# Kernel tuning notes

Measured on AMD Instinct MI355X. Metric: run time of the kernel, lower is better.

## Reference

```python
import jax, jax.numpy as jnp
import numpy as np

N, C, D, H, W = 4, 9, 16, 1024, 1024  # batch, grid channels, grid size, image HxW


def setup_inputs() -> dict:
    key = jax.random.key(0)
    k1, k2, k3, k4 = jax.random.split(key, 4)
    bilateral_grid = jax.random.normal(k1, (N, C, D, D, D), dtype=jnp.float32)
    guidemap = jax.random.uniform(k2, (N, 3, H, W), dtype=jnp.float32)
    conv_w = jax.random.normal(k3, (3, C + 3), dtype=jnp.float32) * 0.1  # 1x1 conv kernel
    conv_b = jax.random.normal(k4, (3,), dtype=jnp.float32) * 0.1
    return {"bilateral_grid": bilateral_grid, "guidemap": guidemap,
            "conv_w": conv_w, "conv_b": conv_b}


def _trilinear_slice(grid, guide):
    # grid: [N, C, D, D, D]; guide: [N, 3, H, W] with values in [0,1]
    n, c, d = grid.shape[0], grid.shape[1], grid.shape[2]
    h, w = guide.shape[2], guide.shape[3]
    grid_flat = grid.reshape(n, c, d * d * d)
    coords = jnp.clip(guide, 0.0, 1.0) * (d - 1)          # [N,3,H,W]
    i0 = jnp.clip(jnp.floor(coords), 0, d - 2).astype(jnp.int32)
    f = coords - i0.astype(coords.dtype)                   # fractional part
    r0, g0, b0 = i0[:, 0], i0[:, 1], i0[:, 2]              # [N,H,W]
    fr, fg, fb = f[:, 0], f[:, 1], f[:, 2]                 # [N,H,W]

    def gather(ir, ig, ib):
        flat = ((ir * d + ig) * d + ib).reshape(n, 1, h * w)
        return jnp.take_along_axis(grid_flat, flat, axis=2)  # [N,C,H*W]

    out = jnp.zeros((n, c, h * w), dtype=grid.dtype)
    for dr in (0, 1):
        for dg in (0, 1):
            for db in (0, 1):
                wgt = ((fr if dr else 1.0 - fr) *
                       (fg if dg else 1.0 - fg) *
                       (fb if db else 1.0 - fb)).reshape(n, 1, h * w)
                out = out + gather(r0 + dr, g0 + dg, b0 + db) * wgt
    return out.reshape(n, c, h, w)


def reference(bilateral_grid, guidemap, conv_w, conv_b):
    res = _trilinear_slice(bilateral_grid, guidemap)       # [N,9,H,W]
    res = jnp.concatenate([res, guidemap], axis=1)         # [N,12,H,W]
    out = jnp.einsum('oi,nihw->nohw', conv_w, res) + conv_b[None, :, None, None]
    return out
```

## Files before the change

kernel.cpp:

```cpp
#include <hip/hip_runtime.h>
#include <hip/hip_bf16.h>

static constexpr int N_ = 4;
static constexpr int C_ = 9;
static constexpr int D_ = 16;
static constexpr int HWp = 1024 * 1024;
static constexpr int CELLS = D_ * D_ * D_;
static constexpr int PT = HWp / 4;
static constexpr int TPB = 512;
static constexpr int BPI = 256;

typedef float f32x4 __attribute__((ext_vector_type(4)));

__device__ __forceinline__ void unpack3(uint2 w, float& x, float& y, float& z) {
    x = __uint_as_float(w.x << 16);
    y = __uint_as_float(w.x & 0xFFFF0000u);
    z = __uint_as_float(w.y << 16);
}

__device__ __forceinline__ float lerp1(float a, float b, float t) {
    return fmaf(b - a, t, a);
}

__global__ __launch_bounds__(256) void fold_kernel(
    const float* __restrict__ grid, const float* __restrict__ cw,
    uint2* __restrict__ folded)
{
    const int idx  = blockIdx.x * 256 + threadIdx.x;
    const int n    = idx >> 12;
    const int cell = idx & (CELLS - 1);
    const float* g = grid + (size_t)n * C_ * CELLS + cell;

    float a0 = 0.f, a1 = 0.f, a2 = 0.f;
#pragma unroll
    for (int c = 0; c < C_; ++c) {
        float v = g[(size_t)c * CELLS];
        a0 = fmaf(cw[c],      v, a0);
        a1 = fmaf(cw[12 + c], v, a1);
        a2 = fmaf(cw[24 + c], v, a2);
    }
    uint2 v;
    v.x = (unsigned)__bfloat16_as_ushort(__float2bfloat16(a0))
        | ((unsigned)__bfloat16_as_ushort(__float2bfloat16(a1)) << 16);
    v.y = (unsigned)__bfloat16_as_ushort(__float2bfloat16(a2));
    folded[idx] = v;
}

__global__ __launch_bounds__(TPB) void slice_kernel(
    const uint2* __restrict__ folded, const float* __restrict__ guide,
    const float* __restrict__ cw, const float* __restrict__ cbias,
    float* __restrict__ out)
{
    __shared__ uint2 sPre[CELLS];

    const int n  = blockIdx.x >> 8;
    const int bi = blockIdx.x & (BPI - 1);

    {
        const uint4* src = (const uint4*)(folded + (size_t)n * CELLS);
        uint4* dst = (uint4*)sPre;
#pragma unroll
        for (int k = 0; k < (CELLS / 2) / TPB; ++k) {
            int i = k * TPB + threadIdx.x;
            dst[i] = src[i];
        }
    }
    __syncthreads();

    const f32x4* gR = (const f32x4*)(guide + (size_t)(n * 3 + 0) * HWp);
    const f32x4* gG = (const f32x4*)(guide + (size_t)(n * 3 + 1) * HWp);
    const f32x4* gB = (const f32x4*)(guide + (size_t)(n * 3 + 2) * HWp);
    f32x4* oR = (f32x4*)(out + (size_t)(n * 3 + 0) * HWp);
    f32x4* oG = (f32x4*)(out + (size_t)(n * 3 + 1) * HWp);
    f32x4* oB = (f32x4*)(out + (size_t)(n * 3 + 2) * HWp);

    const float w0r = cw[9],  w0g = cw[10], w0b = cw[11];
    const float w1r = cw[21], w1g = cw[22], w1b = cw[23];
    const float w2r = cw[33], w2g = cw[34], w2b = cw[35];
    const float bi0 = cbias[0], bi1 = cbias[1], bi2 = cbias[2];

    const int base0 = bi * (PT / BPI);

#pragma unroll
    for (int it = 0; it < (PT / BPI) / TPB; ++it) {
        const int p4 = base0 + it * TPB + threadIdx.x;
        f32x4 r4 = __builtin_nontemporal_load(gR + p4);
        f32x4 g4 = __builtin_nontemporal_load(gG + p4);
        f32x4 b4 = __builtin_nontemporal_load(gB + p4);

        float rr[4] = {r4.x, r4.y, r4.z, r4.w};
        float gg[4] = {g4.x, g4.y, g4.z, g4.w};
        float bb[4] = {b4.x, b4.y, b4.z, b4.w};
        float o0[4], o1[4], o2[4];

#pragma unroll
        for (int j = 0; j < 4; ++j) {
            float cr = fminf(fmaxf(rr[j], 0.f), 1.f) * 15.f;
            float cg = fminf(fmaxf(gg[j], 0.f), 1.f) * 15.f;
            float cb = fminf(fmaxf(bb[j], 0.f), 1.f) * 15.f;
            int ir = min((int)cr, 14);
            int ig = min((int)cg, 14);
            int ib = min((int)cb, 14);
            float fr = cr - (float)ir;
            float fg = cg - (float)ig;
            float fb = cb - (float)ib;
            int base = (ir * 16 + ig) * 16 + ib;

            uint2 q000 = sPre[base];
            uint2 q001 = sPre[base + 1];
            uint2 q010 = sPre[base + 16];
            uint2 q011 = sPre[base + 17];
            uint2 q100 = sPre[base + 256];
            uint2 q101 = sPre[base + 257];
            uint2 q110 = sPre[base + 272];
            uint2 q111 = sPre[base + 273];

            float ax, ay, az, bx, by, bz;
            float v00x, v00y, v00z, v01x, v01y, v01z;
            float v10x, v10y, v10z, v11x, v11y, v11z;

            unpack3(q000, ax, ay, az); unpack3(q001, bx, by, bz);
            v00x = lerp1(ax, bx, fb); v00y = lerp1(ay, by, fb); v00z = lerp1(az, bz, fb);
            unpack3(q010, ax, ay, az); unpack3(q011, bx, by, bz);
            v01x = lerp1(ax, bx, fb); v01y = lerp1(ay, by, fb); v01z = lerp1(az, bz, fb);
            unpack3(q100, ax, ay, az); unpack3(q101, bx, by, bz);
            v10x = lerp1(ax, bx, fb); v10y = lerp1(ay, by, fb); v10z = lerp1(az, bz, fb);
            unpack3(q110, ax, ay, az); unpack3(q111, bx, by, bz);
            v11x = lerp1(ax, bx, fb); v11y = lerp1(ay, by, fb); v11z = lerp1(az, bz, fb);

            float v0x = lerp1(v00x, v01x, fg);
            float v0y = lerp1(v00y, v01y, fg);
            float v0z = lerp1(v00z, v01z, fg);
            float v1x = lerp1(v10x, v11x, fg);
            float v1y = lerp1(v10y, v11y, fg);
            float v1z = lerp1(v10z, v11z, fg);

            float vx = lerp1(v0x, v1x, fr);
            float vy = lerp1(v0y, v1y, fr);
            float vz = lerp1(v0z, v1z, fr);

            o0[j] = vx + fmaf(w0r, rr[j], fmaf(w0g, gg[j], fmaf(w0b, bb[j], bi0)));
            o1[j] = vy + fmaf(w1r, rr[j], fmaf(w1g, gg[j], fmaf(w1b, bb[j], bi1)));
            o2[j] = vz + fmaf(w2r, rr[j], fmaf(w2g, gg[j], fmaf(w2b, bb[j], bi2)));
        }

        f32x4 s0 = {o0[0], o0[1], o0[2], o0[3]};
        f32x4 s1 = {o1[0], o1[1], o1[2], o1[3]};
        f32x4 s2 = {o2[0], o2[1], o2[2], o2[3]};
        __builtin_nontemporal_store(s0, oR + p4);
        __builtin_nontemporal_store(s1, oG + p4);
        __builtin_nontemporal_store(s2, oB + p4);
    }
}

extern "C" void kernel_launch(void* const* d_in, const int* in_sizes, int n_in,
                              void* d_out, int out_size, void* d_ws, size_t ws_size,
                              hipStream_t stream) {
    const float* grid  = (const float*)d_in[0];
    const float* guide = (const float*)d_in[1];
    const float* cw    = (const float*)d_in[2];
    const float* cb    = (const float*)d_in[3];
    float* out = (float*)d_out;
    uint2* folded = (uint2*)d_ws;

    fold_kernel<<<(N_ * CELLS) / 256, 256, 0, stream>>>(grid, cw, folded);
    slice_kernel<<<N_ * BPI, TPB, 0, stream>>>(folded, guide, cw, cb, out);
}
```

Measured before the change: 115.2 us.

## Store b-axis neighbor pairs in folded grid to halve LDS gathers

The fold kernel now writes each cell together with its +1 neighbor along the b axis as one 16-byte record. The slice kernel can then fetch the 8 trilinear corners with 4 uint4 LDS reads instead of 8 uint2 reads. The shared table doubles to 64KB per block, which limits occupancy. To amortize the larger per-block table load, blocks per image drop from 256 to 128, so each block handles more pixels.

```diff
diff --git a/kernel.cpp b/kernel.cpp
--- a/kernel.cpp
+++ b/kernel.cpp
@@ -8,61 +8,79 @@
 static constexpr int CELLS = D_ * D_ * D_;
 static constexpr int PT = HWp / 4;
 static constexpr int TPB = 512;
-static constexpr int BPI = 256;
+static constexpr int BPI = 128;
 
 typedef float f32x4 __attribute__((ext_vector_type(4)));
-
-__device__ __forceinline__ void unpack3(uint2 w, float& x, float& y, float& z) {
-    x = __uint_as_float(w.x << 16);
-    y = __uint_as_float(w.x & 0xFFFF0000u);
-    z = __uint_as_float(w.y << 16);
-}
 
 __device__ __forceinline__ float lerp1(float a, float b, float t) {
     return fmaf(b - a, t, a);
 }
 
+__device__ __forceinline__ unsigned pack2bf(float a, float b) {
+    return (unsigned)__bfloat16_as_ushort(__float2bfloat16(a))
+         | ((unsigned)__bfloat16_as_ushort(__float2bfloat16(b)) << 16);
+}
+
+__device__ __forceinline__ void unpack_lerp(uint4 q, float t,
+                                            float& vx, float& vy, float& vz) {
+    float ax = __uint_as_float(q.x << 16);
+    float ay = __uint_as_float(q.x & 0xFFFF0000u);
+    float az = __uint_as_float(q.y << 16);
+    float bx = __uint_as_float(q.z << 16);
+    float by = __uint_as_float(q.z & 0xFFFF0000u);
+    float bz = __uint_as_float(q.w << 16);
+    vx = lerp1(ax, bx, t);
+    vy = lerp1(ay, by, t);
+    vz = lerp1(az, bz, t);
+}
+
 __global__ __launch_bounds__(256) void fold_kernel(
     const float* __restrict__ grid, const float* __restrict__ cw,
-    uint2* __restrict__ folded)
+    uint4* __restrict__ folded)
 {
     const int idx  = blockIdx.x * 256 + threadIdx.x;
     const int n    = idx >> 12;
     const int cell = idx & (CELLS - 1);
-    const float* g = grid + (size_t)n * C_ * CELLS + cell;
+    const int cellN = ((cell & 15) < 15) ? cell + 1 : cell;
+    const float* g = grid + (size_t)n * C_ * CELLS;
 
     float a0 = 0.f, a1 = 0.f, a2 = 0.f;
+    float c0 = 0.f, c1 = 0.f, c2 = 0.f;
 #pragma unroll
     for (int c = 0; c < C_; ++c) {
-        float v = g[(size_t)c * CELLS];
+        float v = g[(size_t)c * CELLS + cell];
+        float w = g[(size_t)c * CELLS + cellN];
         a0 = fmaf(cw[c],      v, a0);
         a1 = fmaf(cw[12 + c], v, a1);
         a2 = fmaf(cw[24 + c], v, a2);
+        c0 = fmaf(cw[c],      w, c0);
+        c1 = fmaf(cw[12 + c], w, c1);
+        c2 = fmaf(cw[24 + c], w, c2);
     }
-    uint2 v;
-    v.x = (unsigned)__bfloat16_as_ushort(__float2bfloat16(a0))
-        | ((unsigned)__bfloat16_as_ushort(__float2bfloat16(a1)) << 16);
-    v.y = (unsigned)__bfloat16_as_ushort(__float2bfloat16(a2));
-    folded[idx] = v;
+    uint4 o;
+    o.x = pack2bf(a0, a1);
+    o.y = (unsigned)__bfloat16_as_ushort(__float2bfloat16(a2));
+    o.z = pack2bf(c0, c1);
+    o.w = (unsigned)__bfloat16_as_ushort(__float2bfloat16(c2));
+    folded[idx] = o;
 }
 
 __global__ __launch_bounds__(TPB) void slice_kernel(
-    const uint2* __restrict__ folded, const float* __restrict__ guide,
+    const uint4* __restrict__ folded, const float* __restrict__ guide,
     const float* __restrict__ cw, const float* __restrict__ cbias,
     float* __restrict__ out)
 {
-    __shared__ uint2 sPre[CELLS];
+    __shared__ uint4 sPre[CELLS];
 
-    const int n  = blockIdx.x >> 8;
+    const int n  = blockIdx.x >> 7;
     const int bi = blockIdx.x & (BPI - 1);
 
     {
-        const uint4* src = (const uint4*)(folded + (size_t)n * CELLS);
-        uint4* dst = (uint4*)sPre;
+        const uint4* src = folded + (size_t)n * CELLS;
 #pragma unroll
-        for (int k = 0; k < (CELLS / 2) / TPB; ++k) {
+        for (int k = 0; k < CELLS / TPB; ++k) {
             int i = k * TPB + threadIdx.x;
-            dst[i] = src[i];
+            sPre[i] = src[i];
         }
     }
     __syncthreads();
@@ -106,27 +124,17 @@
             float fb = cb - (float)ib;
             int base = (ir * 16 + ig) * 16 + ib;
 
-            uint2 q000 = sPre[base];
-            uint2 q001 = sPre[base + 1];
-            uint2 q010 = sPre[base + 16];
-            uint2 q011 = sPre[base + 17];
-            uint2 q100 = sPre[base + 256];
-            uint2 q101 = sPre[base + 257];
-            uint2 q110 = sPre[base + 272];
-            uint2 q111 = sPre[base + 273];
+            uint4 q00 = sPre[base];
+            uint4 q01 = sPre[base + 16];
+            uint4 q10 = sPre[base + 256];
+            uint4 q11 = sPre[base + 272];
 
-            float ax, ay, az, bx, by, bz;
             float v00x, v00y, v00z, v01x, v01y, v01z;
             float v10x, v10y, v10z, v11x, v11y, v11z;
-
-            unpack3(q000, ax, ay, az); unpack3(q001, bx, by, bz);
-            v00x = lerp1(ax, bx, fb); v00y = lerp1(ay, by, fb); v00z = lerp1(az, bz, fb);
-            unpack3(q010, ax, ay, az); unpack3(q011, bx, by, bz);
-            v01x = lerp1(ax, bx, fb); v01y = lerp1(ay, by, fb); v01z = lerp1(az, bz, fb);
-            unpack3(q100, ax, ay, az); unpack3(q101, bx, by, bz);
-            v10x = lerp1(ax, bx, fb); v10y = lerp1(ay, by, fb); v10z = lerp1(az, bz, fb);
-            unpack3(q110, ax, ay, az); unpack3(q111, bx, by, bz);
-            v11x = lerp1(ax, bx, fb); v11y = lerp1(ay, by, fb); v11z = lerp1(az, bz, fb);
+            unpack_lerp(q00, fb, v00x, v00y, v00z);
+            unpack_lerp(q01, fb, v01x, v01y, v01z);
+            unpack_lerp(q10, fb, v10x, v10y, v10z);
+            unpack_lerp(q11, fb, v11x, v11y, v11z);
 
             float v0x = lerp1(v00x, v01x, fg);
             float v0y = lerp1(v00y, v01y, fg);
@@ -161,7 +169,7 @@
     const float* cw    = (const float*)d_in[2];
     const float* cb    = (const float*)d_in[3];
     float* out = (float*)d_out;
-    uint2* folded = (uint2*)d_ws;
+    uint4* folded = (uint4*)d_ws;
 
     fold_kernel<<<(N_ * CELLS) / 256, 256, 0, stream>>>(grid, cw, folded);
     slice_kernel<<<N_ * BPI, TPB, 0, stream>>>(folded, guide, cw, cb, out);
```

Measured after the change: 113.3 us. Within noise of the previous version (-1.7%).
